# Optimization experiments

Hardware: AMD Instinct MI355X
Metric: run time of the kernel (lower is better)

The kernel has to match this reference:

```python
import jax, jax.numpy as jnp
import numpy as np
from jax import lax

B, C, A = 32, 84, 8400      # batch, 4+nc channels, anchors (640x640, strides 8/16/32)
NC = 80                     # num classes
K = 1000                    # max_det
CONF_THRES = 0.1
IOU_THRES = 0.7
MAX_WH = 7680.0             # class offset for non-agnostic NMS (ultralytics constant)
SCALE = min(640.0 / 1080.0, 640.0 / 1920.0)  # letterbox scale (input 640, orig 1920x1080)


def setup_inputs() -> dict:
    key = jax.random.key(0)
    k1, k2, k3 = jax.random.split(key, 3)
    # YOLOv8 head output: rows 0:4 are decoded xywh boxes in input pixels, rows 4: are sigmoided class scores
    cxcy = jax.random.uniform(k1, (B, 2, A), jnp.float32, 0.0, 640.0)
    wh = jax.random.uniform(k2, (B, 2, A), jnp.float32, 8.0, 120.0)
    scores = jax.random.uniform(k3, (B, NC, A), jnp.float32, 0.0, 1.0)
    preds = jnp.concatenate([cxcy, wh, scores], axis=1)  # [B, 84, A]
    return {"preds": preds}


def _xywh2xyxy(b):
    cx, cy, w, h = b[:, 0], b[:, 1], b[:, 2], b[:, 3]
    return jnp.stack([cx - w / 2, cy - h / 2, cx + w / 2, cy + h / 2], axis=1)


def _pairwise_iou(b):  # b: [K,4] xyxy
    area = (b[:, 2] - b[:, 0]) * (b[:, 3] - b[:, 1])
    lt = jnp.maximum(b[:, None, :2], b[None, :, :2])
    rb = jnp.minimum(b[:, None, 2:], b[None, :, 2:])
    wh = jnp.clip(rb - lt, 0.0)
    inter = wh[..., 0] * wh[..., 1]
    return inter / (area[:, None] + area[None, :] - inter + 1e-7)


def _nms_per_image(p):  # p: [84, A]
    boxes = _xywh2xyxy(p[:4].T)          # [A,4]
    cls_scores = p[4:]                   # [NC, A]
    conf = jnp.max(cls_scores, axis=0)   # best-class confidence (multi_label=False)
    cls = jnp.argmax(cls_scores, axis=0).astype(jnp.float32)
    # conf threshold + class filter (classes=[0])
    valid = (conf > CONF_THRES) & (cls == 0.0)
    masked = jnp.where(valid, conf, -1.0)
    top_s, idx = lax.top_k(masked, K)    # candidates sorted by score desc
    top_boxes = boxes[idx]               # [K,4]
    top_cls = cls[idx]
    top_valid = top_s > CONF_THRES
    # class-offset boxes for non-agnostic NMS (agnostic=False)
    nms_boxes = top_boxes + top_cls[:, None] * MAX_WH
    iou = _pairwise_iou(nms_boxes)       # [K,K]
    ar = jnp.arange(K)

    def body(i, keep):
        suppress = (iou[i] > IOU_THRES) & keep[i] & (ar > i)
        return keep & ~suppress

    keep = lax.fori_loop(0, K, body, top_valid)
    out_boxes = top_boxes / SCALE        # rescale to original image coords
    out = jnp.concatenate(
        [out_boxes, top_s[:, None], top_cls[:, None]], axis=1)  # [K,6]
    return jnp.where(keep[:, None], out, 0.0)


def reference(preds):
    # [B, K, 6]: x1,y1,x2,y2 (original-image coords), score, class
    return jax.vmap(_nms_per_image)(preds)
```

## Files before the change

### kernel.cpp

```cpp
#include <hip/hip_runtime.h>

#define BATCH 32
#define CH    84
#define NA    8400
#define KTOP  1000
#define GROUPS 2100
#define SLICES 33
#define SLOT   32
#define MAXC   (SLICES*SLOT)
#define IOU_T 0.7f

__global__ __launch_bounds__(256) void cand_kernel(const float* __restrict__ preds,
        int* __restrict__ counts, float* __restrict__ cscore, int* __restrict__ cidx) {
    int b = blockIdx.x / SLICES;
    int slice = blockIdx.x - b * SLICES;
    int t = threadIdx.x;
    int w = t >> 6, l = t & 63;
    int g = slice * 64 + l;
    bool active = g < GROUPS;

    __shared__ int lcount;
    __shared__ float4 red[3][64];
    __shared__ float lsc[256];
    __shared__ int   lix[256];
    if (t == 0) lcount = 0;

    const float* base = preds + (size_t)b * (CH * NA);
    float mx = -1.f, my = -1.f, mz = -1.f, mw = -1.f;
    float4 s0 = make_float4(-2.f, -2.f, -2.f, -2.f);
    if (active) {
        int c0 = (w < 3) ? (5 + 20 * w) : 64;
        const float* p = base + (size_t)c0 * NA + 4 * g;
        #pragma unroll
        for (int k = 0; k < 20; ++k, p += NA) {
            float4 v = *(const float4*)p;
            mx = fmaxf(mx, v.x); my = fmaxf(my, v.y);
            mz = fmaxf(mz, v.z); mw = fmaxf(mw, v.w);
        }
        if (w == 0) s0 = *(const float4*)(base + (size_t)4 * NA + 4 * g);
    }
    if (w > 0) red[w - 1][l] = make_float4(mx, my, mz, mw);
    __syncthreads();

    if (w == 0 && active) {
        #pragma unroll
        for (int ww = 0; ww < 3; ++ww) {
            float4 r = red[ww][l];
            mx = fmaxf(mx, r.x); my = fmaxf(my, r.y);
            mz = fmaxf(mz, r.z); mw = fmaxf(mw, r.w);
        }
        float s[4] = {s0.x, s0.y, s0.z, s0.w};
        float m[4] = {mx, my, mz, mw};
        #pragma unroll
        for (int k = 0; k < 4; ++k) {
            if (s[k] > 0.1f && s[k] >= m[k]) {
                int p_ = atomicAdd(&lcount, 1);
                lsc[p_] = s[k];
                lix[p_] = 4 * g + k;
            }
        }
    }
    __syncthreads();
    int n = lcount; if (n > SLOT) n = SLOT;
    if (t == 0) counts[b * SLICES + slice] = n;
    if (t < n) {
        cscore[b * MAXC + slice * SLOT + t] = lsc[t];
        cidx[b * MAXC + slice * SLOT + t]   = lix[t];
    }
}

template<int S>
__device__ unsigned int nms_scan(int n, int lane, const float4* bxy, const float* ars) {
    float ox1[S], oy1[S], ox2[S], oy2[S], oar[S];
    unsigned int keep = 0u;
    #pragma unroll
    for (int k = 0; k < S; ++k) {
        int c = k * 64 + lane;
        if (c < n) {
            float4 v = bxy[c];
            ox1[k] = v.x; oy1[k] = v.y; ox2[k] = v.z; oy2[k] = v.w;
            oar[k] = ars[c];
            keep |= (1u << k);
        } else {
            ox1[k] = 0.f; oy1[k] = 0.f; ox2[k] = -1.f; oy2[k] = -1.f; oar[k] = 0.f;
        }
    }
    for (int i = 0; i < n; ++i) {
        int which = i >> 6, src = i & 63;
        int mybit = (keep >> which) & 1;
        unsigned long long bal = __ballot(mybit);
        if ((bal >> src) & 1ull) {
            float4 bi = bxy[i];
            float ai = ars[i];
            #pragma unroll
            for (int k = 0; k < S; ++k) {
                float lx = fmaxf(bi.x, ox1[k]), ly = fmaxf(bi.y, oy1[k]);
                float rx = fminf(bi.z, ox2[k]), ry = fminf(bi.w, oy2[k]);
                float iw = fmaxf(rx - lx, 0.0f), ih = fmaxf(ry - ly, 0.0f);
                float inter = iw * ih;
                float iou = inter / (ai + oar[k] - inter + 1e-7f);
                int c = k * 64 + lane;
                if (c > i && iou > IOU_T) keep &= ~(1u << k);
            }
        }
    }
    return keep;
}

__global__ __launch_bounds__(256) void nms_kernel(const float* __restrict__ preds,
        const int* __restrict__ counts, const float* __restrict__ cscore,
        const int* __restrict__ cidx, float* __restrict__ out) {
    int b = blockIdx.x;
    int tid = threadIdx.x;

    __shared__ int scnt[SLICES], soff[SLICES + 1];
    __shared__ float rs[MAXC]; __shared__ int ri[MAXC];
    __shared__ float ss[MAXC]; __shared__ int sa[MAXC];
    __shared__ float4 bxy[MAXC];
    __shared__ float  ars[MAXC];
    __shared__ unsigned int keepm[64];

    if (tid < SLICES) scnt[tid] = counts[b * SLICES + tid];
    __syncthreads();
    if (tid == 0) {
        int acc = 0;
        #pragma unroll
        for (int s_ = 0; s_ < SLICES; ++s_) { soff[s_] = acc; acc += scnt[s_]; }
        soff[SLICES] = acc;
    }
    __syncthreads();
    int n = soff[SLICES];

    for (int t = tid; t < SLICES * SLOT; t += 256) {
        int slice = t >> 5, j = t & (SLOT - 1);
        if (j < scnt[slice]) {
            int dst = soff[slice] + j;
            rs[dst] = cscore[b * MAXC + t];
            ri[dst] = cidx[b * MAXC + t];
        }
    }
    __syncthreads();

    for (int i = tid; i < n; i += 256) {
        float si = rs[i]; int ii = ri[i];
        int r = 0;
        for (int j = 0; j < n; ++j) {
            float sj = rs[j]; int ij = ri[j];
            if (sj > si || (sj == si && ij < ii)) r++;
        }
        ss[r] = si; sa[r] = ii;
    }
    __syncthreads();

    const float* base = preds + (size_t)b * (CH * NA);
    for (int i = tid; i < n; i += 256) {
        int a = sa[i];
        float cx = base[a], cy = base[NA + a];
        float w  = base[2 * NA + a], h = base[3 * NA + a];
        float hx = w * 0.5f, hy = h * 0.5f;
        float X1 = cx - hx, Y1 = cy - hy, X2 = cx + hx, Y2 = cy + hy;
        bxy[i] = make_float4(X1, Y1, X2, Y2);
        ars[i] = (X2 - X1) * (Y2 - Y1);
    }
    __syncthreads();

    if (tid < 64) {
        unsigned int kp;
        if (n <= 128)      kp = nms_scan<2>(n, tid, bxy, ars);
        else if (n <= 256) kp = nms_scan<4>(n, tid, bxy, ars);
        else if (n <= 512) kp = nms_scan<8>(n, tid, bxy, ars);
        else               kp = nms_scan<17>(n, tid, bxy, ars);
        keepm[tid] = kp;
    }
    __syncthreads();

    float* ob = out + (size_t)b * KTOP * 6;
    const float SCALEF = (float)(640.0 / 1920.0);
    for (int r = tid; r < KTOP; r += 256) {
        float v0 = 0.f, v1 = 0.f, v2 = 0.f, v3 = 0.f, v4 = 0.f, v5 = 0.f;
        if (r < n && ((keepm[r & 63] >> (r >> 6)) & 1u)) {
            float4 bx = bxy[r];
            v0 = bx.x / SCALEF; v1 = bx.y / SCALEF;
            v2 = bx.z / SCALEF; v3 = bx.w / SCALEF;
            v4 = ss[r]; v5 = 0.0f;
        }
        ob[r * 6 + 0] = v0; ob[r * 6 + 1] = v1; ob[r * 6 + 2] = v2;
        ob[r * 6 + 3] = v3; ob[r * 6 + 4] = v4; ob[r * 6 + 5] = v5;
    }
}

extern "C" void kernel_launch(void* const* d_in, const int* in_sizes, int n_in,
                              void* d_out, int out_size, void* d_ws, size_t ws_size,
                              hipStream_t stream) {
    const float* preds = (const float*)d_in[0];
    float* out = (float*)d_out;

    int*   counts = (int*)d_ws;
    float* cscore = (float*)((char*)d_ws + 16384);
    int*   cidx   = (int*)((char*)d_ws + 16384 + (size_t)BATCH * MAXC * sizeof(float));

    cand_kernel<<<BATCH * SLICES, 256, 0, stream>>>(preds, counts, cscore, cidx);
    nms_kernel<<<BATCH, 256, 0, stream>>>(preds, counts, cscore, cidx, out);
}
```

Baseline: 167.3 us.

## Restructure NMS gather: padded slots, ballot compaction, register broadcast in scan

The candidate kernel now writes fixed padded 32-entry slots with sentinel scores, so the count array goes away. The NMS kernel loads all slots and box coordinates in parallel up front, then compacts them with ballot/popcount instead of a serial prefix over counts. Sorting now records positions rather than moving boxes. In the scan, the current box is broadcast from registers via readlane instead of reloaded from shared memory. Output is written as float4 vectors. The aim is to cut the serialized latency of the single-block-per-image NMS kernel, at the price of more registers and indirect position lookups.

```diff
diff --git a/kernel.cpp b/kernel.cpp
--- a/kernel.cpp
+++ b/kernel.cpp
@@ -11,7 +11,7 @@
 #define IOU_T 0.7f
 
 __global__ __launch_bounds__(256) void cand_kernel(const float* __restrict__ preds,
-        int* __restrict__ counts, float* __restrict__ cscore, int* __restrict__ cidx) {
+        float* __restrict__ cscore, int* __restrict__ cidx) {
     int b = blockIdx.x / SLICES;
     int slice = blockIdx.x - b * SLICES;
     int t = threadIdx.x;
@@ -62,24 +62,30 @@
     }
     __syncthreads();
     int n = lcount; if (n > SLOT) n = SLOT;
-    if (t == 0) counts[b * SLICES + slice] = n;
-    if (t < n) {
-        cscore[b * MAXC + slice * SLOT + t] = lsc[t];
-        cidx[b * MAXC + slice * SLOT + t]   = lix[t];
-    }
+    if (t < SLOT) {
+        int o = b * MAXC + slice * SLOT + t;
+        cscore[o] = (t < n) ? lsc[t] : -1.f;
+        cidx[o]   = (t < n) ? lix[t] : 0;
+    }
+}
+
+__device__ __forceinline__ float bcastf(float v, int src) {
+    return __uint_as_float(__builtin_amdgcn_readlane(__float_as_uint(v), src));
 }
 
 template<int S>
-__device__ unsigned int nms_scan(int n, int lane, const float4* bxy, const float* ars) {
+__device__ unsigned int nms_scan(int n, int lane, const float4* bxy,
+                                 const float* ars, const int* pos) {
     float ox1[S], oy1[S], ox2[S], oy2[S], oar[S];
     unsigned int keep = 0u;
     #pragma unroll
     for (int k = 0; k < S; ++k) {
         int c = k * 64 + lane;
         if (c < n) {
-            float4 v = bxy[c];
+            int p = pos[c];
+            float4 v = bxy[p];
             ox1[k] = v.x; oy1[k] = v.y; ox2[k] = v.z; oy2[k] = v.w;
-            oar[k] = ars[c];
+            oar[k] = ars[p];
             keep |= (1u << k);
         } else {
             ox1[k] = 0.f; oy1[k] = 0.f; ox2[k] = -1.f; oy2[k] = -1.f; oar[k] = 0.f;
@@ -90,15 +96,20 @@
         int mybit = (keep >> which) & 1;
         unsigned long long bal = __ballot(mybit);
         if ((bal >> src) & 1ull) {
-            float4 bi = bxy[i];
-            float ai = ars[i];
+            float sx1 = ox1[0], sy1 = oy1[0], sx2 = ox2[0], sy2 = oy2[0], sar = oar[0];
+            #pragma unroll
+            for (int q = 1; q < S; ++q)
+                if (which == q) { sx1 = ox1[q]; sy1 = oy1[q]; sx2 = ox2[q]; sy2 = oy2[q]; sar = oar[q]; }
+            float bix1 = bcastf(sx1, src), biy1 = bcastf(sy1, src);
+            float bix2 = bcastf(sx2, src), biy2 = bcastf(sy2, src);
+            float bia  = bcastf(sar, src);
             #pragma unroll
             for (int k = 0; k < S; ++k) {
-                float lx = fmaxf(bi.x, ox1[k]), ly = fmaxf(bi.y, oy1[k]);
-                float rx = fminf(bi.z, ox2[k]), ry = fminf(bi.w, oy2[k]);
+                float lx = fmaxf(bix1, ox1[k]), ly = fmaxf(biy1, oy1[k]);
+                float rx = fminf(bix2, ox2[k]), ry = fminf(biy2, oy2[k]);
                 float iw = fmaxf(rx - lx, 0.0f), ih = fmaxf(ry - ly, 0.0f);
                 float inter = iw * ih;
-                float iou = inter / (ai + oar[k] - inter + 1e-7f);
+                float iou = inter / (bia + oar[k] - inter + 1e-7f);
                 int c = k * 64 + lane;
                 if (c > i && iou > IOU_T) keep &= ~(1u << k);
             }
@@ -108,84 +119,115 @@
 }
 
 __global__ __launch_bounds__(256) void nms_kernel(const float* __restrict__ preds,
-        const int* __restrict__ counts, const float* __restrict__ cscore,
-        const int* __restrict__ cidx, float* __restrict__ out) {
+        const float* __restrict__ cscore, const int* __restrict__ cidx,
+        float* __restrict__ out) {
     int b = blockIdx.x;
     int tid = threadIdx.x;
-
-    __shared__ int scnt[SLICES], soff[SLICES + 1];
+    int lane = tid & 63, w = tid >> 6;
+
+    __shared__ unsigned long long masks[20];
+    __shared__ int mbase[20];
+    __shared__ int ntot_s;
     __shared__ float rs[MAXC]; __shared__ int ri[MAXC];
-    __shared__ float ss[MAXC]; __shared__ int sa[MAXC];
     __shared__ float4 bxy[MAXC];
     __shared__ float  ars[MAXC];
+    __shared__ float ss[MAXC];
+    __shared__ int   pos[MAXC];
     __shared__ unsigned int keepm[64];
 
-    if (tid < SLICES) scnt[tid] = counts[b * SLICES + tid];
+    const float* base = preds + (size_t)b * (CH * NA);
+    const float* csb = cscore + (size_t)b * MAXC;
+    const int*   cib = cidx   + (size_t)b * MAXC;
+
+    float sc[5]; int ai[5];
+    #pragma unroll
+    for (int k = 0; k < 5; ++k) {
+        int t = k * 256 + tid;
+        bool in = t < MAXC;
+        sc[k] = in ? csb[t] : -1.f;
+        ai[k] = in ? cib[t] : 0;
+    }
+    float bx1[5], by1[5], bx2[5], by2[5], bar[5];
+    #pragma unroll
+    for (int k = 0; k < 5; ++k) {
+        int a = ai[k];
+        float cx = base[a], cy = base[NA + a];
+        float ww = base[2 * NA + a], hh = base[3 * NA + a];
+        float hx = ww * 0.5f, hy = hh * 0.5f;
+        bx1[k] = cx - hx; by1[k] = cy - hy; bx2[k] = cx + hx; by2[k] = cy + hy;
+        bar[k] = (bx2[k] - bx1[k]) * (by2[k] - by1[k]);
+    }
+    unsigned long long bal[5];
+    #pragma unroll
+    for (int k = 0; k < 5; ++k) {
+        bal[k] = __ballot(sc[k] > 0.f);
+        if (lane == 0) masks[k * 4 + w] = bal[k];
+    }
     __syncthreads();
     if (tid == 0) {
         int acc = 0;
         #pragma unroll
-        for (int s_ = 0; s_ < SLICES; ++s_) { soff[s_] = acc; acc += scnt[s_]; }
-        soff[SLICES] = acc;
-    }
-    __syncthreads();
-    int n = soff[SLICES];
-
-    for (int t = tid; t < SLICES * SLOT; t += 256) {
-        int slice = t >> 5, j = t & (SLOT - 1);
-        if (j < scnt[slice]) {
-            int dst = soff[slice] + j;
-            rs[dst] = cscore[b * MAXC + t];
-            ri[dst] = cidx[b * MAXC + t];
-        }
-    }
-    __syncthreads();
-
-    for (int i = tid; i < n; i += 256) {
-        float si = rs[i]; int ii = ri[i];
-        int r = 0;
-        for (int j = 0; j < n; ++j) {
-            float sj = rs[j]; int ij = ri[j];
-            if (sj > si || (sj == si && ij < ii)) r++;
-        }
-        ss[r] = si; sa[r] = ii;
-    }
-    __syncthreads();
-
-    const float* base = preds + (size_t)b * (CH * NA);
-    for (int i = tid; i < n; i += 256) {
-        int a = sa[i];
-        float cx = base[a], cy = base[NA + a];
-        float w  = base[2 * NA + a], h = base[3 * NA + a];
-        float hx = w * 0.5f, hy = h * 0.5f;
-        float X1 = cx - hx, Y1 = cy - hy, X2 = cx + hx, Y2 = cy + hy;
-        bxy[i] = make_float4(X1, Y1, X2, Y2);
-        ars[i] = (X2 - X1) * (Y2 - Y1);
+        for (int m = 0; m < 20; ++m) { mbase[m] = acc; acc += __popcll(masks[m]); }
+        ntot_s = acc;
+    }
+    __syncthreads();
+    unsigned long long lmask = (1ull << lane) - 1ull;
+    #pragma unroll
+    for (int k = 0; k < 5; ++k) {
+        if (sc[k] > 0.f) {
+            int dst = mbase[k * 4 + w] + __popcll(bal[k] & lmask);
+            rs[dst] = sc[k]; ri[dst] = ai[k];
+            bxy[dst] = make_float4(bx1[k], by1[k], bx2[k], by2[k]);
+            ars[dst] = bar[k];
+        }
+    }
+    __syncthreads();
+    int n = __builtin_amdgcn_readfirstlane(ntot_s);
+
+    #pragma unroll
+    for (int k = 0; k < 5; ++k) {
+        int i = k * 256 + tid;
+        if (i < n) {
+            float si = rs[i]; int ii = ri[i];
+            int r = 0;
+            for (int j = 0; j < n; ++j) {
+                float sj = rs[j]; int ij = ri[j];
+                if (sj > si || (sj == si && ij < ii)) r++;
+            }
+            ss[r] = si; pos[r] = i;
+        }
     }
     __syncthreads();
 
     if (tid < 64) {
         unsigned int kp;
-        if (n <= 128)      kp = nms_scan<2>(n, tid, bxy, ars);
-        else if (n <= 256) kp = nms_scan<4>(n, tid, bxy, ars);
-        else if (n <= 512) kp = nms_scan<8>(n, tid, bxy, ars);
-        else               kp = nms_scan<17>(n, tid, bxy, ars);
+        if (n <= 128)      kp = nms_scan<2>(n, tid, bxy, ars, pos);
+        else if (n <= 256) kp = nms_scan<4>(n, tid, bxy, ars, pos);
+        else if (n <= 512) kp = nms_scan<8>(n, tid, bxy, ars, pos);
+        else               kp = nms_scan<17>(n, tid, bxy, ars, pos);
         keepm[tid] = kp;
     }
     __syncthreads();
 
-    float* ob = out + (size_t)b * KTOP * 6;
+    float* ob = out + (size_t)b * (KTOP * 6);
     const float SCALEF = (float)(640.0 / 1920.0);
-    for (int r = tid; r < KTOP; r += 256) {
-        float v0 = 0.f, v1 = 0.f, v2 = 0.f, v3 = 0.f, v4 = 0.f, v5 = 0.f;
-        if (r < n && ((keepm[r & 63] >> (r >> 6)) & 1u)) {
-            float4 bx = bxy[r];
-            v0 = bx.x / SCALEF; v1 = bx.y / SCALEF;
-            v2 = bx.z / SCALEF; v3 = bx.w / SCALEF;
-            v4 = ss[r]; v5 = 0.0f;
-        }
-        ob[r * 6 + 0] = v0; ob[r * 6 + 1] = v1; ob[r * 6 + 2] = v2;
-        ob[r * 6 + 3] = v3; ob[r * 6 + 4] = v4; ob[r * 6 + 5] = v5;
+    for (int q = tid; q < (KTOP * 6) / 4; q += 256) {
+        float4 v;
+        #pragma unroll
+        for (int c = 0; c < 4; ++c) {
+            int f = q * 4 + c;
+            int r = f / 6, cc = f - r * 6;
+            float val = 0.f;
+            if (r < n && ((keepm[r & 63] >> (r >> 6)) & 1u)) {
+                if (cc == 4) val = ss[r];
+                else if (cc < 4) {
+                    const float* bp = (const float*)&bxy[pos[r]];
+                    val = bp[cc] / SCALEF;
+                }
+            }
+            ((float*)&v)[c] = val;
+        }
+        *(float4*)(ob + 4 * q) = v;
     }
 }
 
@@ -195,10 +237,9 @@
     const float* preds = (const float*)d_in[0];
     float* out = (float*)d_out;
 
-    int*   counts = (int*)d_ws;
-    float* cscore = (float*)((char*)d_ws + 16384);
-    int*   cidx   = (int*)((char*)d_ws + 16384 + (size_t)BATCH * MAXC * sizeof(float));
-
-    cand_kernel<<<BATCH * SLICES, 256, 0, stream>>>(preds, counts, cscore, cidx);
-    nms_kernel<<<BATCH, 256, 0, stream>>>(preds, counts, cscore, cidx, out);
-}
+    float* cscore = (float*)d_ws;
+    int*   cidx   = (int*)((char*)d_ws + (size_t)BATCH * MAXC * sizeof(float));
+
+    cand_kernel<<<BATCH * SLICES, 256, 0, stream>>>(preds, cscore, cidx);
+    nms_kernel<<<BATCH, 256, 0, stream>>>(preds, cscore, cidx, out);
+}
```

Measured after the change: 166.8 us. About the same (-0.3%).
